# Kernel tuning notes

Hardware: AMD Instinct MI355X
Metric: run time of the kernel (lower is better)

## Reference

```python
import jax, jax.numpy as jnp
import numpy as np

H = 1024        # hidden_size
I = 2048        # intermediate_size
E = 8           # num_experts
K = 2           # num_experts_per_tok
AUX_COEF = 0.01
Z_COEF = 0.001


def setup_inputs() -> dict:
    key = jax.random.key(0)
    ks = jax.random.split(key, 8)
    s = 0.02
    return {
        "hidden_states": jax.random.normal(ks[0], (1, 2048, H), dtype=jnp.float32),
        "router_w": jax.random.normal(ks[1], (H, E), dtype=jnp.float32) * s,
        "eg": jax.random.normal(ks[2], (E, H, I), dtype=jnp.float32) * s,  # gate_proj per expert
        "eu": jax.random.normal(ks[3], (E, H, I), dtype=jnp.float32) * s,  # up_proj per expert
        "ed": jax.random.normal(ks[4], (E, I, H), dtype=jnp.float32) * s,  # down_proj per expert
        "sg": jax.random.normal(ks[5], (H, I), dtype=jnp.float32) * s,     # shared expert gate
        "su": jax.random.normal(ks[6], (H, I), dtype=jnp.float32) * s,     # shared expert up
        "sd": jax.random.normal(ks[7], (I, H), dtype=jnp.float32) * s,     # shared expert down
    }


def reference(hidden_states, router_w, eg, eu, ed, sg, su, sd):
    B, S, _ = hidden_states.shape
    x = hidden_states.reshape(-1, H)  # [T, H]

    # shared expert (num_shared_experts = 1)
    shared = (jax.nn.silu(x @ sg) * (x @ su)) @ sd  # [T, H]

    # router: linear -> softmax -> top-k, renormalize top-k probs
    logits = x @ router_w                      # [T, E]
    probs = jax.nn.softmax(logits, axis=-1)
    topw, topi = jax.lax.top_k(probs, K)       # [T, K]
    topw = topw / jnp.sum(topw, axis=-1, keepdims=True)

    # combine weights [T, E]: weight of expert e for token t (0 if not routed)
    combine = jnp.sum(jax.nn.one_hot(topi, E, dtype=x.dtype) * topw[..., None], axis=1)

    # dense expert compute (mathematically identical to masked gather/scatter loop)
    g = jnp.einsum('th,ehi->eti', x, eg)       # [E, T, I]
    u = jnp.einsum('th,ehi->eti', x, eu)
    h = jax.nn.silu(g) * u
    expert_out = jnp.einsum('eti,eih->eth', h, ed)  # [E, T, H]
    routed = jnp.einsum('eth,te->th', expert_out, combine)

    output = (shared + routed).reshape(B, S, H)

    # aux losses: Switch-style load balancing + router z-loss
    f = jnp.mean(jax.nn.one_hot(topi, E, dtype=x.dtype), axis=(0, 1))  # fraction dispatched
    p = jnp.mean(probs, axis=0)                                        # mean router prob
    lb_loss = AUX_COEF * E * jnp.sum(f * p)
    z_loss = Z_COEF * jnp.mean(jax.nn.logsumexp(logits, axis=-1) ** 2)
    aux_loss = lb_loss + z_loss
    return output, aux_loss
```

## Files before the change

kernel.cpp:

```cpp
#include <hip/hip_runtime.h>
#include <hip/hip_bf16.h>
#include <stdint.h>

#define T_ 2048
#define H_ 1024
#define I_ 2048
#define E_ 8
#define NE_ 9

typedef __attribute__((ext_vector_type(8))) short bf16x8;
typedef __attribute__((ext_vector_type(4))) float f32x4;

__device__ __forceinline__ unsigned short f2bf(float f) {
  unsigned int u; __builtin_memcpy(&u, &f, 4);
  u = (u + 0x7fffu + ((u >> 16) & 1u)) >> 16;
  return (unsigned short)u;
}
__device__ __forceinline__ void cvt2(float a, float b, unsigned short* dst) {
  __hip_bfloat162 h = __float22bfloat162_rn(float2{a, b});
  __builtin_memcpy(dst, &h, 4);
}
__device__ __forceinline__ void gll16(const void* g, void* l) {
  __builtin_amdgcn_global_load_lds((const __attribute__((address_space(1))) void*)g,
                                   (__attribute__((address_space(3))) void*)l, 16, 0, 0);
}

__global__ __launch_bounds__(256) void k_pack(
    const float* __restrict__ eg, const float* __restrict__ eu, const float* __restrict__ ed,
    const float* __restrict__ sg, const float* __restrict__ su, const float* __restrict__ sd,
    unsigned short* __restrict__ wgp, unsigned short* __restrict__ wup,
    unsigned short* __restrict__ wdp) {
  int kt = blockIdx.x, nt = blockIdx.y, z = blockIdx.z;
  int grp = z / NE_, e = z % NE_;
  int K = (grp == 2) ? I_ : H_;
  int N = (grp == 2) ? H_ : I_;
  if (kt * 32 >= K || nt * 64 >= N) return;
  const float* src; unsigned short* dst;
  if (grp == 0)      { src = (e < E_) ? eg + (size_t)e * H_ * I_ : sg; dst = wgp + (size_t)e * H_ * I_; }
  else if (grp == 1) { src = (e < E_) ? eu + (size_t)e * H_ * I_ : su; dst = wup + (size_t)e * H_ * I_; }
  else               { src = (e < E_) ? ed + (size_t)e * I_ * H_ : sd; dst = wdp + (size_t)e * I_ * H_; }

  __shared__ __align__(16) float lds[32 * 68];
  int t = threadIdx.x;
  const float* srcbase = src + (size_t)(kt * 32) * N + nt * 64;
  int r0 = t >> 4, c0 = (t & 15) * 4;
  float4 v0 = *(const float4*)(srcbase + (size_t)r0 * N + c0);
  float4 v1 = *(const float4*)(srcbase + (size_t)(r0 + 16) * N + c0);
  *(float4*)&lds[r0 * 68 + c0] = v0;
  *(float4*)&lds[(r0 + 16) * 68 + c0] = v1;
  __syncthreads();

  int q = t >> 6, nn = t & 63;
  unsigned short o[8];
#pragma unroll
  for (int j = 0; j < 8; j += 2) {
    float a = lds[(q * 8 + j) * 68 + nn];
    float b = lds[(q * 8 + j + 1) * 68 + nn];
    cvt2(a, b, &o[j]);
  }
  size_t tile = ((size_t)nt * (K / 32) + kt) * 2048;
  *(bf16x8*)&dst[tile + q * 512 + nn * 8] = *(bf16x8*)o;
}

__global__ __launch_bounds__(256) void k_router(
    const float* __restrict__ x, const float* __restrict__ rw,
    int* __restrict__ topi, float* __restrict__ topw,
    float* __restrict__ probs, float* __restrict__ lse2) {
  __shared__ float lrw[E_ * H_];
  int tid = threadIdx.x;
#pragma unroll
  for (int i = 0; i < 8; i++) {
    int idx = i * 256 + tid;
    float4 v = ((const float4*)rw)[idx];
    int f = idx * 4; int h = f >> 3; int e0 = f & 7;
    lrw[(e0 + 0) * H_ + h] = v.x;
    lrw[(e0 + 1) * H_ + h] = v.y;
    lrw[(e0 + 2) * H_ + h] = v.z;
    lrw[(e0 + 3) * H_ + h] = v.w;
  }
  __syncthreads();
  int w = tid >> 6, lane = tid & 63;
  int t = blockIdx.x * 4 + w;
  const float* xp = x + (size_t)t * H_ + lane;
  float xr[16];
#pragma unroll
  for (int j = 0; j < 16; j++) xr[j] = xp[j * 64];
  float acc[E_];
#pragma unroll
  for (int e = 0; e < E_; e++) acc[e] = 0.f;
#pragma unroll
  for (int j = 0; j < 16; j++) {
    float xf = xr[j];
    const float* wp = &lrw[j * 64 + lane];
#pragma unroll
    for (int e = 0; e < E_; e++) acc[e] += xf * wp[e * H_];
  }
#pragma unroll
  for (int off = 32; off >= 1; off >>= 1) {
#pragma unroll
    for (int e = 0; e < E_; e++) acc[e] += __shfl_xor(acc[e], off, 64);
  }
  if (lane == 0) {
    float m = acc[0];
#pragma unroll
    for (int e = 1; e < E_; e++) m = fmaxf(m, acc[e]);
    float p[E_], s = 0.f;
#pragma unroll
    for (int e = 0; e < E_; e++) { p[e] = expf(acc[e] - m); s += p[e]; }
    float inv = 1.f / s;
#pragma unroll
    for (int e = 0; e < E_; e++) p[e] *= inv;
    float lse = m + logf(s);
    lse2[t] = lse * lse;
    float4 p0 = {p[0], p[1], p[2], p[3]}, p1 = {p[4], p[5], p[6], p[7]};
    ((float4*)(probs + t * 8))[0] = p0;
    ((float4*)(probs + t * 8))[1] = p1;
    int i0 = 0;
#pragma unroll
    for (int e = 1; e < E_; e++) if (p[e] > p[i0]) i0 = e;
    int i1 = (i0 == 0) ? 1 : 0;
#pragma unroll
    for (int e = 0; e < E_; e++) if (e != i0 && e != i1 && p[e] > p[i1]) i1 = e;
    float w0 = p[i0], w1 = p[i1], wsum = w0 + w1;
    topi[t * 2] = i0; topi[t * 2 + 1] = i1;
    topw[t * 2] = w0 / wsum; topw[t * 2 + 1] = w1 / wsum;
  }
}

__global__ __launch_bounds__(256) void k_reduce(
    const float* __restrict__ probs, const float* __restrict__ lse2,
    const int* __restrict__ topi,
    int* cnt, int* poffs, float* out_aux) {
  __shared__ float sp[256][9];
  __shared__ int sc[256][8];
  int tid = threadIdx.x;
  float ps[9] = {0.f, 0.f, 0.f, 0.f, 0.f, 0.f, 0.f, 0.f, 0.f};
  int c[8] = {0, 0, 0, 0, 0, 0, 0, 0};
  for (int t = tid; t < T_; t += 256) {
#pragma unroll
    for (int e = 0; e < E_; e++) ps[e] += probs[t * 8 + e];
    ps[8] += lse2[t];
    c[topi[t * 2]]++; c[topi[t * 2 + 1]]++;
  }
#pragma unroll
  for (int e = 0; e < 9; e++) sp[tid][e] = ps[e];
#pragma unroll
  for (int e = 0; e < 8; e++) sc[tid][e] = c[e];
  __syncthreads();
  for (int s = 128; s > 0; s >>= 1) {
    if (tid < s) {
#pragma unroll
      for (int e = 0; e < 9; e++) sp[tid][e] += sp[tid + s][e];
#pragma unroll
      for (int e = 0; e < 8; e++) sc[tid][e] += sc[tid + s][e];
    }
    __syncthreads();
  }
  if (tid == 0) {
#pragma unroll
    for (int e = 0; e < E_; e++) cnt[e] = sc[0][e];
    cnt[E_] = T_;
    int po = 0;
    for (int e = 0; e < NE_; e++) { poffs[e] = po; po += ((cnt[e] + 127) >> 7) << 7; }
    poffs[NE_] = po;
    float lb = 0.f;
#pragma unroll
    for (int e = 0; e < E_; e++)
      lb += ((float)cnt[e] / 4096.f) * (sp[0][e] / 2048.f);
    out_aux[0] = 0.01f * 8.f * lb + 0.001f * (sp[0][8] / 2048.f);
  }
}

__global__ __launch_bounds__(256) void k_fill(
    const int* __restrict__ topi, const float* __restrict__ topw,
    const int* __restrict__ poffs, int* cur, int* tok, float* wgt) {
  __shared__ int hist[8];
  __shared__ int base[8];
  int tid = threadIdx.x;
  int t = blockIdx.x * 256 + tid;
  if (tid < 8) hist[tid] = 0;
  __syncthreads();
  int e0 = topi[t * 2], e1 = topi[t * 2 + 1];
  int p0 = atomicAdd(&hist[e0], 1);
  int p1 = atomicAdd(&hist[e1], 1);
  __syncthreads();
  if (tid < 8) base[tid] = atomicAdd(&cur[tid], hist[tid]);
  __syncthreads();
  tok[poffs[e0] + base[e0] + p0] = t; wgt[poffs[e0] + base[e0] + p0] = topw[t * 2];
  tok[poffs[e1] + base[e1] + p1] = t; wgt[poffs[e1] + base[e1] + p1] = topw[t * 2 + 1];
  int p8 = poffs[E_];
  tok[p8 + t] = t;
  wgt[p8 + t] = 1.f;
}

__global__ __launch_bounds__(256) void k_packA(
    const float* __restrict__ x, const int* __restrict__ cnt,
    const int* __restrict__ poffs, const int* __restrict__ tok,
    unsigned short* __restrict__ apack) {
  int kc = blockIdx.x, mt = blockIdx.y, e = blockIdx.z;
  int cnt_e = cnt[e];
  if (mt * 128 >= cnt_e) return;
  int po = poffs[e];
  int rt = (po >> 7) + mt;
  int t = threadIdx.x;
  int m = t & 127, qh = t >> 7;
  int atok = tok[po + min(mt * 128 + m, cnt_e - 1)];
  const float* arow = x + (size_t)atok * H_;
  size_t abase = (size_t)rt * 32 * 4096;
#pragma unroll
  for (int ki = 0; ki < 4; ki++) {
    int kt = kc * 4 + ki;
#pragma unroll
    for (int qo = 0; qo < 2; qo++) {
      int q = qh + qo * 2;
      const float* s = arow + kt * 32 + q * 8;
      float4 v0 = *(const float4*)s, v1 = *(const float4*)(s + 4);
      unsigned short t8[8];
      cvt2(v0.x, v0.y, t8); cvt2(v0.z, v0.w, t8 + 2);
      cvt2(v1.x, v1.y, t8 + 4); cvt2(v1.z, v1.w, t8 + 6);
      *(bf16x8*)&apack[abase + (size_t)kt * 4096 + q * 1024 + m * 8] = *(bf16x8*)t8;
    }
  }
}

#define G1_GRID 1792
__global__ __launch_bounds__(256) void k_gemm1(
    const unsigned short* __restrict__ apack,
    const unsigned short* __restrict__ wgp, const unsigned short* __restrict__ wup,
    const int* __restrict__ cnt, const int* __restrict__ poffs,
    unsigned short* __restrict__ hbuf) {
  int lin = blockIdx.x;
  int s = (lin & 7) * (G1_GRID / 8) + (lin >> 3);
  int rt = s >> 5, nt = s & 31;
  int rtTotal = poffs[NE_] >> 7;
  if (rt >= rtTotal) return;
  int ro = rt << 7;
  int e = 0;
#pragma unroll
  for (int i = 1; i < NE_; i++) if (poffs[i] <= ro) e = i;
  int po = poffs[e];
  int cnt_e = cnt[e];
  int mt = (ro - po) >> 7;

  __shared__ __align__(16) unsigned short As[2][4096];
  __shared__ __align__(16) unsigned short BgS[2][2048];
  __shared__ __align__(16) unsigned short BuS[2][2048];

  int tid = threadIdx.x;
  int lane = tid & 63, w = tid >> 6;
  int quad = lane >> 4, l15 = lane & 15;
  int wm = w >> 1, wn = w & 1;

  const unsigned short* abase = apack + (size_t)rt * 32 * 4096;
  const unsigned short* bgb = wgp + (size_t)e * H_ * I_ + (size_t)nt * 32 * 2048;
  const unsigned short* bub = wup + (size_t)e * H_ * I_ + (size_t)nt * 32 * 2048;

  f32x4 zero = {0.f, 0.f, 0.f, 0.f};
  f32x4 accg[4][2], accu[4][2];
#pragma unroll
  for (int mi = 0; mi < 4; mi++)
#pragma unroll
    for (int ni = 0; ni < 2; ni++) { accg[mi][ni] = zero; accu[mi][ni] = zero; }

#define STAGE1(kt, b) do { \
    const unsigned short* asrc = abase + (size_t)(kt) * 4096 + w * 1024 + lane * 8; \
    gll16(asrc, &As[b][w * 1024]); \
    gll16(asrc + 512, &As[b][w * 1024 + 512]); \
    gll16(bgb + (size_t)(kt) * 2048 + w * 512 + lane * 8, &BgS[b][w * 512]); \
    gll16(bub + (size_t)(kt) * 2048 + w * 512 + lane * 8, &BuS[b][w * 512]); \
  } while (0)

  STAGE1(0, 0);
  __syncthreads();
  for (int kt = 0; kt < 32; kt++) {
    int cur = kt & 1;
    if (kt < 31) STAGE1(kt + 1, cur ^ 1);
    bf16x8 af[4];
#pragma unroll
    for (int mi = 0; mi < 4; mi++)
      af[mi] = *(const bf16x8*)&As[cur][quad * 1024 + (wm * 64 + mi * 16 + l15) * 8];
#pragma unroll
    for (int ni = 0; ni < 2; ni++) {
      bf16x8 bg = *(const bf16x8*)&BgS[cur][quad * 512 + (wn * 32 + ni * 16 + l15) * 8];
      bf16x8 bu = *(const bf16x8*)&BuS[cur][quad * 512 + (wn * 32 + ni * 16 + l15) * 8];
#pragma unroll
      for (int mi = 0; mi < 4; mi++) {
        accg[mi][ni] = __builtin_amdgcn_mfma_f32_16x16x32_bf16(af[mi], bg, accg[mi][ni], 0, 0, 0);
        accu[mi][ni] = __builtin_amdgcn_mfma_f32_16x16x32_bf16(af[mi], bu, accu[mi][ni], 0, 0, 0);
      }
    }
    __syncthreads();
  }
#undef STAGE1

  size_t hbase = (size_t)rt * 64 * 4096;
  int rem = cnt_e - mt * 128;
#pragma unroll
  for (int ni = 0; ni < 2; ni++) {
    int cc = nt * 64 + wn * 32 + ni * 16 + l15;
    size_t cb = hbase + (size_t)(cc >> 5) * 4096 + (size_t)((cc >> 3) & 3) * 1024 + (cc & 7);
#pragma unroll
    for (int mi = 0; mi < 4; mi++)
#pragma unroll
      for (int r = 0; r < 4; r++) {
        int row = wm * 64 + mi * 16 + quad * 4 + r;
        if (row < rem) {
          float g = accg[mi][ni][r], u = accu[mi][ni][r];
          float sv = g / (1.f + __expf(-g));
          hbuf[cb + (size_t)row * 8] = f2bf(sv * u);
        }
      }
  }
}

#define G2_GRID 1792
__global__ __launch_bounds__(256) void k_gemm2(
    const unsigned short* __restrict__ hbuf, const unsigned short* __restrict__ wdp,
    const int* __restrict__ cnt, const int* __restrict__ poffs,
    const int* __restrict__ tok, const float* __restrict__ wgt,
    float* __restrict__ out) {
  int lin = blockIdx.x;
  int s = (lin & 7) * (G2_GRID / 8) + (lin >> 3);
  int rt = s >> 5;
  int r5 = s & 31;
  int nt = r5 >> 2, kh = r5 & 3;
  int rtTotal = poffs[NE_] >> 7;
  if (rt >= rtTotal) return;
  int ro = rt << 7;
  int e = 0;
#pragma unroll
  for (int i = 1; i < NE_; i++) if (poffs[i] <= ro) e = i;
  int po = poffs[e];
  int cnt_e = cnt[e];
  int mt = (ro - po) >> 7;

  __shared__ __align__(16) unsigned short As[2][4096];
  __shared__ __align__(16) unsigned short BdS[2][4096];

  int tid = threadIdx.x;
  int lane = tid & 63, w = tid >> 6;
  int quad = lane >> 4, l15 = lane & 15;
  int wm = w >> 1, wn = w & 1;

  const unsigned short* abase = hbuf + (size_t)rt * 64 * 4096;
  const unsigned short* bb0 = wdp + (size_t)e * I_ * H_ + ((size_t)(2 * nt) * 64) * 2048;
  const unsigned short* bb1 = wdp + (size_t)e * I_ * H_ + ((size_t)(2 * nt + 1) * 64) * 2048;

  f32x4 zero = {0.f, 0.f, 0.f, 0.f};
  f32x4 acc[4][4];
#pragma unroll
  for (int mi = 0; mi < 4; mi++)
#pragma unroll
    for (int ni = 0; ni < 4; ni++) acc[mi][ni] = zero;

#define STAGE2(kt, b) do { \
    const unsigned short* asrc = abase + (size_t)(kt) * 4096 + w * 1024 + lane * 8; \
    gll16(asrc, &As[b][w * 1024]); \
    gll16(asrc + 512, &As[b][w * 1024 + 512]); \
    gll16(bb0 + (size_t)(kt) * 2048 + w * 512 + lane * 8, &BdS[b][w * 512]); \
    gll16(bb1 + (size_t)(kt) * 2048 + w * 512 + lane * 8, &BdS[b][2048 + w * 512]); \
  } while (0)

  int k0 = kh * 16;
  STAGE2(k0, 0);
  __syncthreads();
  for (int kk = 0; kk < 16; kk++) {
    int cur = kk & 1;
    if (kk < 15) STAGE2(k0 + kk + 1, cur ^ 1);
    bf16x8 af[4];
#pragma unroll
    for (int mi = 0; mi < 4; mi++)
      af[mi] = *(const bf16x8*)&As[cur][quad * 1024 + (wm * 64 + mi * 16 + l15) * 8];
#pragma unroll
    for (int ni = 0; ni < 4; ni++) {
      bf16x8 bd = *(const bf16x8*)&BdS[cur][wn * 2048 + quad * 512 + (ni * 16 + l15) * 8];
#pragma unroll
      for (int mi = 0; mi < 4; mi++)
        acc[mi][ni] = __builtin_amdgcn_mfma_f32_16x16x32_bf16(af[mi], bd, acc[mi][ni], 0, 0, 0);
    }
    __syncthreads();
  }
#undef STAGE2

  int rem = cnt_e - mt * 128;
#pragma unroll
  for (int mi = 0; mi < 4; mi++)
#pragma unroll
    for (int r = 0; r < 4; r++) {
      int row = wm * 64 + mi * 16 + quad * 4 + r;
      if (row < rem) {
        int g = po + mt * 128 + row;
        int tt = tok[g];
        float wt = wgt[g];
#pragma unroll
        for (int ni = 0; ni < 4; ni++) {
          int col = nt * 128 + wn * 64 + ni * 16 + l15;
          atomicAdd(&out[(size_t)tt * H_ + col], wt * acc[mi][ni][r]);
        }
      }
    }
}

extern "C" void kernel_launch(void* const* d_in, const int* in_sizes, int n_in,
                              void* d_out, int out_size, void* d_ws, size_t ws_size,
                              hipStream_t stream) {
  const float* x  = (const float*)d_in[0];
  const float* rw = (const float*)d_in[1];
  const float* eg = (const float*)d_in[2];
  const float* eu = (const float*)d_in[3];
  const float* ed = (const float*)d_in[4];
  const float* sg = (const float*)d_in[5];
  const float* su = (const float*)d_in[6];
  const float* sd = (const float*)d_in[7];
  float* out = (float*)d_out;
  char* ws = (char*)d_ws;

  int*   cnt  = (int*)(ws + 64);
  int*   poffs= (int*)(ws + 128);
  int*   cur  = (int*)(ws + 256);
  int*   topi = (int*)(ws + 4096);
  float* topw = (float*)(ws + 4096 + 16384);
  int*   tok  = (int*)(ws + 36864);
  float* wgt  = (float*)(ws + 66560);
  unsigned short* apack = (unsigned short*)(ws + 131072);
  unsigned short* hbuf  = (unsigned short*)(ws + 131072 + 14811136);
  float* probs = (float*)(ws + 44302336);
  float* lse2  = (float*)(ws + 44367872);
  unsigned short* wgp   = (unsigned short*)(ws + 131072 + 14811136 + 29491200);
  unsigned short* wup   = (unsigned short*)((char*)wgp + (size_t)NE_ * H_ * I_ * 2);
  unsigned short* wdp   = (unsigned short*)((char*)wup + (size_t)NE_ * H_ * I_ * 2);

  hipMemsetAsync(ws, 0, 4096, stream);
  hipMemsetAsync(out, 0, (size_t)T_ * H_ * 4, stream);

  dim3 gp(64, 32, 3 * NE_);
  k_pack<<<gp, 256, 0, stream>>>(eg, eu, ed, sg, su, sd, wgp, wup, wdp);
  k_router<<<512, 256, 0, stream>>>(x, rw, topi, topw, probs, lse2);
  k_reduce<<<1, 256, 0, stream>>>(probs, lse2, topi, cnt, poffs, out + (size_t)T_ * H_);
  k_fill<<<8, 256, 0, stream>>>(topi, topw, poffs, cur, tok, wgt);
  dim3 ga(8, 16, NE_);
  k_packA<<<ga, 256, 0, stream>>>(x, cnt, poffs, tok, apack);
  k_gemm1<<<G1_GRID, 256, 0, stream>>>(apack, wgp, wup, cnt, poffs, hbuf);
  k_gemm2<<<G2_GRID, 256, 0, stream>>>(hbuf, wdp, cnt, poffs, tok, wgt, out);
}
```

Before: 468.8 us.

## Triple-buffer GEMM pipelines, halve gemm2 split-K, fuse fill and memsets

Both expert GEMMs move from double-buffered LDS staging with full __syncthreads to a three-stage ring. It uses explicit vmcnt waits and bare barriers, so loads for the tile two steps ahead overlap the current MFMA work. gemm2 cuts its split-K factor from 4 to 2, halving the grid and the atomic adds into the output at the cost of a longer K loop per block. The router kernel now zeroes the output, replacing the memsets, and the token-fill step is folded into the single-block reduce kernel, which removes launches but serializes the fill in one block.

```diff
diff --git a/kernel.cpp b/kernel.cpp
--- a/kernel.cpp
+++ b/kernel.cpp
@@ -65,9 +65,16 @@
 __global__ __launch_bounds__(256) void k_router(
     const float* __restrict__ x, const float* __restrict__ rw,
     int* __restrict__ topi, float* __restrict__ topw,
-    float* __restrict__ probs, float* __restrict__ lse2) {
+    float* __restrict__ probs, float* __restrict__ lse2,
+    float* __restrict__ outz) {
+  int tid = threadIdx.x;
+  {
+    float4 zf = {0.f, 0.f, 0.f, 0.f};
+    float4* ob = (float4*)(outz + (size_t)blockIdx.x * 4096);
+#pragma unroll
+    for (int i = 0; i < 4; i++) ob[i * 256 + tid] = zf;
+  }
   __shared__ float lrw[E_ * H_];
-  int tid = threadIdx.x;
 #pragma unroll
   for (int i = 0; i < 8; i++) {
     int idx = i * 256 + tid;
@@ -127,12 +134,15 @@
   }
 }
 
-__global__ __launch_bounds__(256) void k_reduce(
+__global__ __launch_bounds__(256) void k_sched(
     const float* __restrict__ probs, const float* __restrict__ lse2,
-    const int* __restrict__ topi,
-    int* cnt, int* poffs, float* out_aux) {
+    const int* __restrict__ topi, const float* __restrict__ topw,
+    int* cnt, int* poffs, float* out_aux,
+    int* __restrict__ tok, float* __restrict__ wgt) {
   __shared__ float sp[256][9];
   __shared__ int sc[256][8];
+  __shared__ int sbase[NE_];
+  __shared__ int scur[8];
   int tid = threadIdx.x;
   float ps[9] = {0.f, 0.f, 0.f, 0.f, 0.f, 0.f, 0.f, 0.f, 0.f};
   int c[8] = {0, 0, 0, 0, 0, 0, 0, 0};
@@ -161,36 +171,28 @@
     for (int e = 0; e < E_; e++) cnt[e] = sc[0][e];
     cnt[E_] = T_;
     int po = 0;
-    for (int e = 0; e < NE_; e++) { poffs[e] = po; po += ((cnt[e] + 127) >> 7) << 7; }
+    for (int e = 0; e < NE_; e++) {
+      poffs[e] = po; sbase[e] = po;
+      int ce = (e < E_) ? sc[0][e] : T_;
+      po += ((ce + 127) >> 7) << 7;
+    }
     poffs[NE_] = po;
     float lb = 0.f;
 #pragma unroll
     for (int e = 0; e < E_; e++)
-      lb += ((float)cnt[e] / 4096.f) * (sp[0][e] / 2048.f);
+      lb += ((float)sc[0][e] / 4096.f) * (sp[0][e] / 2048.f);
     out_aux[0] = 0.01f * 8.f * lb + 0.001f * (sp[0][8] / 2048.f);
   }
-}
-
-__global__ __launch_bounds__(256) void k_fill(
-    const int* __restrict__ topi, const float* __restrict__ topw,
-    const int* __restrict__ poffs, int* cur, int* tok, float* wgt) {
-  __shared__ int hist[8];
-  __shared__ int base[8];
-  int tid = threadIdx.x;
-  int t = blockIdx.x * 256 + tid;
-  if (tid < 8) hist[tid] = 0;
+  if (tid < 8) scur[tid] = 0;
   __syncthreads();
-  int e0 = topi[t * 2], e1 = topi[t * 2 + 1];
-  int p0 = atomicAdd(&hist[e0], 1);
-  int p1 = atomicAdd(&hist[e1], 1);
-  __syncthreads();
-  if (tid < 8) base[tid] = atomicAdd(&cur[tid], hist[tid]);
-  __syncthreads();
-  tok[poffs[e0] + base[e0] + p0] = t; wgt[poffs[e0] + base[e0] + p0] = topw[t * 2];
-  tok[poffs[e1] + base[e1] + p1] = t; wgt[poffs[e1] + base[e1] + p1] = topw[t * 2 + 1];
-  int p8 = poffs[E_];
-  tok[p8 + t] = t;
-  wgt[p8 + t] = 1.f;
+  for (int t = tid; t < T_; t += 256) {
+    int e0 = topi[t * 2], e1 = topi[t * 2 + 1];
+    int p0 = atomicAdd(&scur[e0], 1);
+    int p1 = atomicAdd(&scur[e1], 1);
+    tok[sbase[e0] + p0] = t; wgt[sbase[e0] + p0] = topw[t * 2];
+    tok[sbase[e1] + p1] = t; wgt[sbase[e1] + p1] = topw[t * 2 + 1];
+    tok[sbase[E_] + t] = t; wgt[sbase[E_] + t] = 1.f;
+  }
 }
 
 __global__ __launch_bounds__(256) void k_packA(
@@ -242,9 +244,9 @@
   int cnt_e = cnt[e];
   int mt = (ro - po) >> 7;
 
-  __shared__ __align__(16) unsigned short As[2][4096];
-  __shared__ __align__(16) unsigned short BgS[2][2048];
-  __shared__ __align__(16) unsigned short BuS[2][2048];
+  __shared__ __align__(16) unsigned short As[3][4096];
+  __shared__ __align__(16) unsigned short BgS[3][2048];
+  __shared__ __align__(16) unsigned short BuS[3][2048];
 
   int tid = threadIdx.x;
   int lane = tid & 63, w = tid >> 6;
@@ -270,28 +272,40 @@
     gll16(bub + (size_t)(kt) * 2048 + w * 512 + lane * 8, &BuS[b][w * 512]); \
   } while (0)
 
-  STAGE1(0, 0);
-  __syncthreads();
-  for (int kt = 0; kt < 32; kt++) {
-    int cur = kt & 1;
-    if (kt < 31) STAGE1(kt + 1, cur ^ 1);
-    bf16x8 af[4];
-#pragma unroll
-    for (int mi = 0; mi < 4; mi++)
-      af[mi] = *(const bf16x8*)&As[cur][quad * 1024 + (wm * 64 + mi * 16 + l15) * 8];
-#pragma unroll
-    for (int ni = 0; ni < 2; ni++) {
-      bf16x8 bg = *(const bf16x8*)&BgS[cur][quad * 512 + (wn * 32 + ni * 16 + l15) * 8];
-      bf16x8 bu = *(const bf16x8*)&BuS[cur][quad * 512 + (wn * 32 + ni * 16 + l15) * 8];
-#pragma unroll
-      for (int mi = 0; mi < 4; mi++) {
-        accg[mi][ni] = __builtin_amdgcn_mfma_f32_16x16x32_bf16(af[mi], bg, accg[mi][ni], 0, 0, 0);
-        accu[mi][ni] = __builtin_amdgcn_mfma_f32_16x16x32_bf16(af[mi], bu, accu[mi][ni], 0, 0, 0);
-      }
-    }
-    __syncthreads();
-  }
+#define COMP1(b) do { \
+    bf16x8 af[4]; \
+    _Pragma("unroll") \
+    for (int mi = 0; mi < 4; mi++) \
+      af[mi] = *(const bf16x8*)&As[b][quad * 1024 + (wm * 64 + mi * 16 + l15) * 8]; \
+    _Pragma("unroll") \
+    for (int ni = 0; ni < 2; ni++) { \
+      bf16x8 bg = *(const bf16x8*)&BgS[b][quad * 512 + (wn * 32 + ni * 16 + l15) * 8]; \
+      bf16x8 bu = *(const bf16x8*)&BuS[b][quad * 512 + (wn * 32 + ni * 16 + l15) * 8]; \
+      _Pragma("unroll") \
+      for (int mi = 0; mi < 4; mi++) { \
+        accg[mi][ni] = __builtin_amdgcn_mfma_f32_16x16x32_bf16(af[mi], bg, accg[mi][ni], 0, 0, 0); \
+        accu[mi][ni] = __builtin_amdgcn_mfma_f32_16x16x32_bf16(af[mi], bu, accu[mi][ni], 0, 0, 0); \
+      } \
+    } \
+  } while (0)
+
+#define WAIT4 asm volatile("s_waitcnt vmcnt(4)" ::: "memory")
+#define WAIT0 asm volatile("s_waitcnt vmcnt(0)" ::: "memory")
+#define BAR __builtin_amdgcn_s_barrier()
+
+  STAGE1(0, 0); STAGE1(1, 1);
+  WAIT4; BAR;
+  for (int it = 0; it < 10; ++it) {
+    int kt = it * 3;
+    STAGE1(kt + 2, 2); COMP1(0); WAIT4; BAR;
+    STAGE1(kt + 3, 0); COMP1(1); WAIT4; BAR;
+    STAGE1(kt + 4, 1); COMP1(2); WAIT4; BAR;
+  }
+  COMP1(0);
+  WAIT0; BAR;
+  COMP1(1);
 #undef STAGE1
+#undef COMP1
 
   size_t hbase = (size_t)rt * 64 * 4096;
   int rem = cnt_e - mt * 128;
@@ -313,7 +327,7 @@
   }
 }
 
-#define G2_GRID 1792
+#define G2_GRID 896
 __global__ __launch_bounds__(256) void k_gemm2(
     const unsigned short* __restrict__ hbuf, const unsigned short* __restrict__ wdp,
     const int* __restrict__ cnt, const int* __restrict__ poffs,
@@ -321,9 +335,9 @@
     float* __restrict__ out) {
   int lin = blockIdx.x;
   int s = (lin & 7) * (G2_GRID / 8) + (lin >> 3);
-  int rt = s >> 5;
-  int r5 = s & 31;
-  int nt = r5 >> 2, kh = r5 & 3;
+  int rt = s >> 4;
+  int r4 = s & 15;
+  int nt = r4 >> 1, kh = r4 & 1;
   int rtTotal = poffs[NE_] >> 7;
   if (rt >= rtTotal) return;
   int ro = rt << 7;
@@ -334,14 +348,15 @@
   int cnt_e = cnt[e];
   int mt = (ro - po) >> 7;
 
-  __shared__ __align__(16) unsigned short As[2][4096];
-  __shared__ __align__(16) unsigned short BdS[2][4096];
+  __shared__ __align__(16) unsigned short As[3][4096];
+  __shared__ __align__(16) unsigned short BdS[3][4096];
 
   int tid = threadIdx.x;
   int lane = tid & 63, w = tid >> 6;
   int quad = lane >> 4, l15 = lane & 15;
   int wm = w >> 1, wn = w & 1;
 
+  int k0 = kh * 32;
   const unsigned short* abase = hbuf + (size_t)rt * 64 * 4096;
   const unsigned short* bb0 = wdp + (size_t)e * I_ * H_ + ((size_t)(2 * nt) * 64) * 2048;
   const unsigned short* bb1 = wdp + (size_t)e * I_ * H_ + ((size_t)(2 * nt + 1) * 64) * 2048;
@@ -353,34 +368,41 @@
 #pragma unroll
     for (int ni = 0; ni < 4; ni++) acc[mi][ni] = zero;
 
-#define STAGE2(kt, b) do { \
-    const unsigned short* asrc = abase + (size_t)(kt) * 4096 + w * 1024 + lane * 8; \
+#define STAGE2(kk, b) do { \
+    const unsigned short* asrc = abase + (size_t)(k0 + (kk)) * 4096 + w * 1024 + lane * 8; \
     gll16(asrc, &As[b][w * 1024]); \
     gll16(asrc + 512, &As[b][w * 1024 + 512]); \
-    gll16(bb0 + (size_t)(kt) * 2048 + w * 512 + lane * 8, &BdS[b][w * 512]); \
-    gll16(bb1 + (size_t)(kt) * 2048 + w * 512 + lane * 8, &BdS[b][2048 + w * 512]); \
+    gll16(bb0 + (size_t)(k0 + (kk)) * 2048 + w * 512 + lane * 8, &BdS[b][w * 512]); \
+    gll16(bb1 + (size_t)(k0 + (kk)) * 2048 + w * 512 + lane * 8, &BdS[b][2048 + w * 512]); \
   } while (0)
 
-  int k0 = kh * 16;
-  STAGE2(k0, 0);
-  __syncthreads();
-  for (int kk = 0; kk < 16; kk++) {
-    int cur = kk & 1;
-    if (kk < 15) STAGE2(k0 + kk + 1, cur ^ 1);
-    bf16x8 af[4];
-#pragma unroll
-    for (int mi = 0; mi < 4; mi++)
-      af[mi] = *(const bf16x8*)&As[cur][quad * 1024 + (wm * 64 + mi * 16 + l15) * 8];
-#pragma unroll
-    for (int ni = 0; ni < 4; ni++) {
-      bf16x8 bd = *(const bf16x8*)&BdS[cur][wn * 2048 + quad * 512 + (ni * 16 + l15) * 8];
-#pragma unroll
-      for (int mi = 0; mi < 4; mi++)
-        acc[mi][ni] = __builtin_amdgcn_mfma_f32_16x16x32_bf16(af[mi], bd, acc[mi][ni], 0, 0, 0);
-    }
-    __syncthreads();
-  }
+#define COMP2(b) do { \
+    bf16x8 af[4]; \
+    _Pragma("unroll") \
+    for (int mi = 0; mi < 4; mi++) \
+      af[mi] = *(const bf16x8*)&As[b][quad * 1024 + (wm * 64 + mi * 16 + l15) * 8]; \
+    _Pragma("unroll") \
+    for (int ni = 0; ni < 4; ni++) { \
+      bf16x8 bd = *(const bf16x8*)&BdS[b][wn * 2048 + quad * 512 + (ni * 16 + l15) * 8]; \
+      _Pragma("unroll") \
+      for (int mi = 0; mi < 4; mi++) \
+        acc[mi][ni] = __builtin_amdgcn_mfma_f32_16x16x32_bf16(af[mi], bd, acc[mi][ni], 0, 0, 0); \
+    } \
+  } while (0)
+
+  STAGE2(0, 0); STAGE2(1, 1);
+  WAIT4; BAR;
+  for (int it = 0; it < 10; ++it) {
+    int kk = it * 3;
+    STAGE2(kk + 2, 2); COMP2(0); WAIT4; BAR;
+    STAGE2(kk + 3, 0); COMP2(1); WAIT4; BAR;
+    STAGE2(kk + 4, 1); COMP2(2); WAIT4; BAR;
+  }
+  COMP2(0);
+  WAIT0; BAR;
+  COMP2(1);
 #undef STAGE2
+#undef COMP2
 
   int rem = cnt_e - mt * 128;
 #pragma unroll
@@ -417,7 +439,6 @@
 
   int*   cnt  = (int*)(ws + 64);
   int*   poffs= (int*)(ws + 128);
-  int*   cur  = (int*)(ws + 256);
   int*   topi = (int*)(ws + 4096);
   float* topw = (float*)(ws + 4096 + 16384);
   int*   tok  = (int*)(ws + 36864);
@@ -430,14 +451,11 @@
   unsigned short* wup   = (unsigned short*)((char*)wgp + (size_t)NE_ * H_ * I_ * 2);
   unsigned short* wdp   = (unsigned short*)((char*)wup + (size_t)NE_ * H_ * I_ * 2);
 
-  hipMemsetAsync(ws, 0, 4096, stream);
-  hipMemsetAsync(out, 0, (size_t)T_ * H_ * 4, stream);
-
   dim3 gp(64, 32, 3 * NE_);
   k_pack<<<gp, 256, 0, stream>>>(eg, eu, ed, sg, su, sd, wgp, wup, wdp);
-  k_router<<<512, 256, 0, stream>>>(x, rw, topi, topw, probs, lse2);
-  k_reduce<<<1, 256, 0, stream>>>(probs, lse2, topi, cnt, poffs, out + (size_t)T_ * H_);
-  k_fill<<<8, 256, 0, stream>>>(topi, topw, poffs, cur, tok, wgt);
+  k_router<<<512, 256, 0, stream>>>(x, rw, topi, topw, probs, lse2, out);
+  k_sched<<<1, 256, 0, stream>>>(probs, lse2, topi, topw, cnt, poffs,
+                                 out + (size_t)T_ * H_, tok, wgt);
   dim3 ga(8, 16, NE_);
   k_packA<<<ga, 256, 0, stream>>>(x, cnt, poffs, tok, apack);
   k_gemm1<<<G1_GRID, 256, 0, stream>>>(apack, wgp, wup, cnt, poffs, hbuf);
```

After: 438.5 us. -6.5%, faster.
